# Optimization experiments

Hardware: AMD Instinct MI355X
Metric: run time of the kernel (lower is better)

The kernel has to match this reference:

```python
import jax, jax.numpy as jnp
import numpy as np

H = 128        # hidden_size
E = 128        # embedding_size
D = 2 * H      # num_directions * hidden_size
B = 512        # batch
T = 100        # n_cities == max_time_steps
MID = 100
STD = 0.1


def _p(k, shape):
    return STD * jax.random.normal(k, shape, dtype=jnp.float32)


def setup_inputs():
    ks = jax.random.split(jax.random.key(0), 22)
    return {
        "inputs": jax.random.normal(ks[0], (B, T, 2), dtype=jnp.float32),
        "W_embed": _p(ks[1], (E, 2)),
        "enc_Wih_f": _p(ks[2], (4 * H, E)),
        "enc_Whh_f": _p(ks[3], (4 * H, H)),
        "enc_b_f": _p(ks[4], (4 * H,)),
        "enc_Wih_b": _p(ks[5], (4 * H, E)),
        "enc_Whh_b": _p(ks[6], (4 * H, H)),
        "enc_b_b": _p(ks[7], (4 * H,)),
        "W_ref": _p(ks[8], (D, D)),
        "W_q": _p(ks[9], (D, D)),
        "v_w": _p(ks[10], (D,)),
        "v_b": _p(ks[11], (1,)),
        "proc_Wih_f": _p(ks[12], (4 * H, D)),
        "proc_Whh_f": _p(ks[13], (4 * H, H)),
        "proc_b_f": _p(ks[14], (4 * H,)),
        "proc_Wih_b": _p(ks[15], (4 * H, D)),
        "proc_Whh_b": _p(ks[16], (4 * H, H)),
        "proc_b_b": _p(ks[17], (4 * H,)),
        "W1": _p(ks[18], (MID, D)),
        "b1": _p(ks[19], (MID,)),
        "W2": _p(ks[20], (1, MID)),
        "b2": _p(ks[21], (1,)),
    }


def _cell(x, h, c, Wih, Whh, b):
    # PyTorch LSTM gate order: i, f, g, o
    gates = x @ Wih.T + h @ Whh.T + b
    i, f, g, o = jnp.split(gates, 4, axis=-1)
    c2 = jax.nn.sigmoid(f) * c + jax.nn.sigmoid(i) * jnp.tanh(g)
    h2 = jax.nn.sigmoid(o) * jnp.tanh(c2)
    return h2, c2


def _lstm_dir(xs, Wih, Whh, b):
    # xs: [T, B, in] -> (hs [T,B,H], h_last [B,H], c_last [B,H])
    bsz = xs.shape[1]
    h0 = jnp.zeros((bsz, H), xs.dtype)

    def step(carry, x):
        h, c = carry
        h, c = _cell(x, h, c, Wih, Whh, b)
        return (h, c), h

    (h, c), hs = jax.lax.scan(step, (h0, h0), xs)
    return hs, h, c


def _forward(inputs, W_embed, enc_Wih_f, enc_Whh_f, enc_b_f, enc_Wih_b, enc_Whh_b,
             enc_b_b, W_ref, W_q, v_w, v_b, proc_Wih_f, proc_Whh_f, proc_b_f,
             proc_Wih_b, proc_Whh_b, proc_b_b, W1, b1, W2, b2, remat=False):
    bsz, city, _ = inputs.shape
    emb = inputs @ W_embed.T                      # [B, T, E]
    xs = emb.transpose(1, 0, 2)                   # [T, B, E]
    hs_f, hf, cf = _lstm_dir(xs, enc_Wih_f, enc_Whh_f, enc_b_f)
    hs_b, hb, cb = _lstm_dir(xs[::-1], enc_Wih_b, enc_Whh_b, enc_b_b)
    enc = jnp.concatenate([hs_f, hs_b[::-1]], axis=-1).transpose(1, 0, 2)  # [B, T, D]
    ref = enc @ W_ref.T                           # loop-invariant W_ref(Enc): [B, T, D]

    def step(carry, _):
        pin, shf, scf, shb, scb = carry
        # bidirectional LSTM over a length-1 sequence = two independent cells
        shf, scf = _cell(pin, shf, scf, proc_Wih_f, proc_Whh_f, proc_b_f)
        shb, scb = _cell(pin, shb, scb, proc_Wih_b, proc_Whh_b, proc_b_b)
        pout = jnp.concatenate([shf, shb], axis=-1)              # [B, D]
        scores = jnp.tanh(ref + (pout @ W_q.T)[:, None, :]) @ v_w + v_b[0]  # [B, T]
        attn = jax.nn.softmax(scores, axis=1)
        pin = jnp.einsum('bt,btd->bd', attn, enc)                # glimpse
        return (pin, shf, scf, shb, scb), pout

    if remat:
        step = jax.checkpoint(step)

    pin0 = jnp.zeros((bsz, D), inputs.dtype)
    _, pouts = jax.lax.scan(step, (pin0, hf, cf, hb, cb), None, length=city)
    pout = pouts[-1]                              # processor_output of last step
    hidden = jax.nn.relu(pout @ W1.T + b1)
    return jnp.squeeze(hidden @ W2.T + b2)        # [B]


def reference(inputs, W_embed, enc_Wih_f, enc_Whh_f, enc_b_f, enc_Wih_b, enc_Whh_b,
              enc_b_b, W_ref, W_q, v_w, v_b, proc_Wih_f, proc_Whh_f, proc_b_f,
              proc_Wih_b, proc_Whh_b, proc_b_b, W1, b1, W2, b2):
    return _forward(inputs, W_embed, enc_Wih_f, enc_Whh_f, enc_b_f, enc_Wih_b,
                    enc_Whh_b, enc_b_b, W_ref, W_q, v_w, v_b, proc_Wih_f,
                    proc_Whh_f, proc_b_f, proc_Wih_b, proc_Whh_b, proc_b_b,
                    W1, b1, W2, b2)
```

## Files before the change

### kernel.cpp

```cpp
#include <hip/hip_runtime.h>


constexpr int kH = 128, kE = 128, kD = 256, kB = 512, kT = 100, kG = 512, kMID = 100;

typedef _Float16 half2_t __attribute__((ext_vector_type(2)));

constexpr size_t WS_ENCH  = 0;
constexpr size_t WS_REFTH = WS_ENCH  + (size_t)kB * kT * kD/2;
constexpr size_t WS_EW2   = WS_REFTH + (size_t)kB * kD * kT/2;
constexpr size_t WS_ECG   = WS_EW2   + 65536;
constexpr size_t WS_PW2   = WS_ECG   + 4096;
constexpr size_t WS_PB    = WS_PW2   + 196608;
constexpr size_t WS_WQ2   = WS_PB    + 1024;
constexpr size_t WS_WREFT = WS_WQ2   + 32768;
constexpr size_t WS_HST   = WS_WREFT + (size_t)kD * kD;
constexpr size_t WS_POUT  = WS_HST   + (size_t)4 * kB * kH;

__device__ __forceinline__ float rcpf(float x) { return __builtin_amdgcn_rcpf(x); }
__device__ __forceinline__ float sigf(float x) { return rcpf(1.0f + __expf(-x)); }
__device__ __forceinline__ float tanhf_(float x) {
    float t = __expf(2.0f * x);
    return 1.0f - 2.0f * rcpf(1.0f + t);
}
__device__ __forceinline__ float fdot2(half2_t a, half2_t b, float c) {
#if __has_builtin(__builtin_amdgcn_fdot2)
    return __builtin_amdgcn_fdot2(a, b, c, false);
#else
    return c + (float)a.x * (float)b.x + (float)a.y * (float)b.y;
#endif
}

__global__ void k_prep_ec(const float* __restrict__ Wih_f, const float* __restrict__ Wih_b,
                          const float* __restrict__ b_f, const float* __restrict__ b_b,
                          const float* __restrict__ Wemb, float* __restrict__ ws) {
    int id = blockIdx.x * 256 + threadIdx.x;
    int dir = id >> 9, j = id & 511;
    const float* Wih = dir ? Wih_b : Wih_f;
    const float* bb  = dir ? b_b   : b_f;
    float c0 = 0.f, c1 = 0.f;
    for (int e = 0; e < kE; ++e) {
        float w = Wih[j * kE + e];
        c0 += w * Wemb[e * 2 + 0];
        c1 += w * Wemb[e * 2 + 1];
    }
    float* ecg = ws + WS_ECG + (size_t)id * 4;
    ecg[0] = c0; ecg[1] = c1; ecg[2] = bb[j]; ecg[3] = 0.f;
}

__global__ void k_prep_tr(const float* __restrict__ eWhh_f, const float* __restrict__ eWhh_b,
                          const float* __restrict__ pWih_f, const float* __restrict__ pWih_b,
                          const float* __restrict__ pWhh_f, const float* __restrict__ pWhh_b,
                          const float* __restrict__ pb_f, const float* __restrict__ pb_b,
                          const float* __restrict__ Wq, const float* __restrict__ Wref,
                          float* __restrict__ ws) {
    int id = blockIdx.x * 256 + threadIdx.x;
    if (id < 65536) {
        int dir = id >> 15, rem = id & 32767, kp = rem >> 9, j = rem & 511;
        const float* W = dir ? eWhh_b : eWhh_f;
        half2_t v = {(_Float16)W[j * kH + 2 * kp], (_Float16)W[j * kH + 2 * kp + 1]};
        ((half2_t*)(ws + WS_EW2))[id] = v;
        return;
    }
    id -= 65536;
    if (id < 196608) {
        int kp = id >> 10, j = id & 1023;
        int k0 = 2 * kp, k1 = 2 * kp + 1;
        float a, b;
        if (k0 < 256) {
            a = (j < 512) ? pWih_f[j * kD + k0] : pWih_b[(j - 512) * kD + k0];
            b = (j < 512) ? pWih_f[j * kD + k1] : pWih_b[(j - 512) * kD + k1];
        } else {
            a = (j < 512) ? pWhh_f[j * kH + (k0 - 256)] : pWhh_b[(j - 512) * kH + (k0 - 256)];
            b = (j < 512) ? pWhh_f[j * kH + (k1 - 256)] : pWhh_b[(j - 512) * kH + (k1 - 256)];
        }
        half2_t v = {(_Float16)a, (_Float16)b};
        ((half2_t*)(ws + WS_PW2))[id] = v;
        return;
    }
    id -= 196608;
    if (id < 1024) {
        ws[WS_PB + id] = (id < 512) ? pb_f[id] : pb_b[id - 512];
        return;
    }
    id -= 1024;
    if (id < 32768) {
        int kp = id >> 8, n = id & 255;
        half2_t v = {(_Float16)Wq[n * kD + 2 * kp], (_Float16)Wq[n * kD + 2 * kp + 1]};
        ((half2_t*)(ws + WS_WQ2))[id] = v;
        return;
    }
    id -= 32768;
    if (id < 65536) {
        int k = id >> 8, n = id & 255;
        ws[WS_WREFT + id] = Wref[n * kD + k];
        return;
    }
}

__global__ __launch_bounds__(512, 2) void k_encoder(const float* __restrict__ inp,
                                                    float* __restrict__ ws) {
    const int dir = blockIdx.x & 1;
    const int b0  = (blockIdx.x >> 1) * 4;
    const int tid = threadIdx.x;
    const int jq  = tid & 127;
    const int kg  = tid >> 7;
    __shared__ __align__(16) half2_t shT2[64][4];
    __shared__ float scs[4][kH];
    __shared__ __align__(16) float uniE[4 * 4 * 512];
    __shared__ __align__(16) float4 secg[512];
    __shared__ float sx[4][2];
    if (tid < 256) ((float*)shT2)[tid] = 0.f;
    if (tid < 512) scs[tid >> 7][tid & 127] = 0.f;
    secg[tid] = *(const float4*)(ws + WS_ECG + (size_t)(dir * 512 + tid) * 4);
    const float4* EW2f4 = (const float4*)(ws + WS_EW2) + (size_t)dir * 64 * 128;
    _Float16* ench = (_Float16*)(ws + WS_ENCH);
    float* hst = ws + WS_HST;
    float4* uniE4 = (float4*)uniE;
    float4 wregE[16];
    #pragma unroll
    for (int i = 0; i < 16; ++i) wregE[i] = EW2f4[(kg * 16 + i) * 128 + jq];
    __syncthreads();
    for (int s = 0; s < kT; ++s) {
        const int t = dir ? (kT - 1 - s) : s;
        if (tid < 8) { int r = tid >> 1, c = tid & 1; sx[r][c] = inp[((size_t)(b0 + r) * kT + t) * 2 + c]; }
        {
            float aa[16];
            #pragma unroll
            for (int i = 0; i < 16; ++i) aa[i] = 0.f;
            #pragma unroll
            for (int kk = 0; kk < 16; ++kk) {
                int kp = kg * 16 + kk;
                float4 xraw = *(const float4*)&shT2[kp][0];
                const half2_t* wp = (const half2_t*)&wregE[kk];
                const half2_t* xp = (const half2_t*)&xraw;
                #pragma unroll
                for (int j = 0; j < 4; ++j)
                    #pragma unroll
                    for (int r = 0; r < 4; ++r)
                        aa[j * 4 + r] = fdot2(wp[j], xp[r], aa[j * 4 + r]);
            }
            #pragma unroll
            for (int r = 0; r < 4; ++r)
                uniE4[(kg * 4 + r) * 128 + jq] = make_float4(aa[0*4+r], aa[1*4+r], aa[2*4+r], aa[3*4+r]);
        }
        __syncthreads();
        {
            const int r = tid >> 7, k = tid & 127;
            float4 c0 = secg[k], c1 = secg[128 + k], c2 = secg[256 + k], c3 = secg[384 + k];
            float x0 = sx[r][0], x1 = sx[r][1];
            float gi = c0.z + x0 * c0.x + x1 * c0.y;
            float gf = c1.z + x0 * c1.x + x1 * c1.y;
            float gg = c2.z + x0 * c2.x + x1 * c2.y;
            float go = c3.z + x0 * c3.x + x1 * c3.y;
            #pragma unroll
            for (int g4 = 0; g4 < 4; ++g4) {
                const float* u = &uniE[(g4 * 4 + r) * 512];
                gi += u[k]; gf += u[k + 128]; gg += u[k + 256]; go += u[k + 384];
            }
            float cc = sigf(gf) * scs[r][k] + sigf(gi) * tanhf_(gg);
            float hh = sigf(go) * tanhf_(cc);
            scs[r][k] = cc;
            ((_Float16*)shT2)[((k >> 1) * 4 + r) * 2 + (k & 1)] = (_Float16)hh;
            ench[((size_t)(b0 + r) * kT + t) * kD + dir * kH + k] = (_Float16)hh;
            if (s == kT - 1) {
                hst[(size_t)(dir * 2 + 0) * kB * kH + (size_t)(b0 + r) * kH + k] = hh;
                hst[(size_t)(dir * 2 + 1) * kB * kH + (size_t)(b0 + r) * kH + k] = cc;
            }
        }
        __syncthreads();
    }
}

__global__ __launch_bounds__(256) void k_refgemm(float* __restrict__ ws) {
    const int tid = threadIdx.x;
    const int m0 = blockIdx.x * 20;
    const int b = m0 / kT, t0 = m0 % kT;
    __shared__ float se[20][kD];
    __shared__ float so[20][257];
    const _Float16* ench = (const _Float16*)(ws + WS_ENCH);
    const float* WrT = ws + WS_WREFT;
    _Float16* refTh = (_Float16*)(ws + WS_REFTH);
    #pragma unroll
    for (int i = 0; i < 20; ++i) se[i][tid] = (float)ench[(size_t)(m0 + i) * kD + tid];
    __syncthreads();
    float acc[20];
    #pragma unroll
    for (int r = 0; r < 20; ++r) acc[r] = 0.f;
    #pragma unroll 2
    for (int k = 0; k < kD; ++k) {
        float w = WrT[k * kD + tid];
        #pragma unroll
        for (int r = 0; r < 20; ++r) acc[r] += se[r][k] * w;
    }
    #pragma unroll
    for (int r = 0; r < 20; ++r) so[r][tid] = acc[r];
    __syncthreads();
    #pragma unroll
    for (int i = 0; i < 20; ++i) {
        int idx = i * 256 + tid;
        int d = idx / 20, tt = idx - d * 20;
        refTh[(size_t)b * kD * kT + d * kT + t0 + tt] = (_Float16)so[tt][d];
    }
}

__global__ __launch_bounds__(1024) void k_process(const float* __restrict__ vw,
                                                  const float* __restrict__ vb,
                                                  float* __restrict__ ws) {
    const int tid = threadIdx.x;
    const int b0 = blockIdx.x * 2;
    __shared__ __align__(16) half2_t xh2[2][192][2];
    __shared__ float pc[2][2][kH];
    __shared__ float hfp[2][2][kH];
    __shared__ __align__(16) float uni[8192];
    __shared__ float qv[2][kD];
    __shared__ float at[2][128];
    __shared__ float vwS[kD];
    __shared__ float sbias[1024];
    const float* PB   = ws + WS_PB;
    const _Float16* refTh = (const _Float16*)(ws + WS_REFTH);
    const _Float16* ench  = (const _Float16*)(ws + WS_ENCH);
    const float* hst  = ws + WS_HST;
    const float4* PW2f4 = (const float4*)(ws + WS_PW2);
    const float*  WQ2f  = ws + WS_WQ2;
    _Float16* xf = (_Float16*)xh2;
    if (tid < 512) {
        int zjh = tid >> 8, zkp = (tid >> 1) & 127, zr = tid & 1;
        ((float*)xh2)[(zjh * 192 + zkp) * 2 + zr] = 0.f;
    }
    if (tid < 512) {
        int r = tid >> 8, dirk = tid & 255, dir = dirk >> 7, k = dirk & 127;
        float hv = hst[(size_t)(dir * 2 + 0) * kB * kH + (size_t)(b0 + r) * kH + k];
        pc[dir][r][k]  = hst[(size_t)(dir * 2 + 1) * kB * kH + (size_t)(b0 + r) * kH + k];
        hfp[dir][r][k] = hv;
        xf[((dir * 192 + 128 + (k >> 1)) * 2 + r) * 2 + (k & 1)] = (_Float16)hv;
    }
    if (tid < kD) vwS[tid] = vw[tid];
    sbias[tid] = PB[tid];
    const float vbias = vb[0];
    const int jq = tid & 255;
    const int kg = tid >> 8;
    const int jh = (jq >= 128);
    float4* uni4 = (float4*)uni;
    __syncthreads();

    for (int step = 0; step < kT; ++step) {
        {
            float a00=0,a01=0,a02=0,a03=0, a10=0,a11=0,a12=0,a13=0;
            #pragma unroll 8
            for (int kk = 0; kk < 48; ++kk) {
                int kp = kg * 48 + kk;
                float4 wraw = PW2f4[(size_t)kp * 256 + jq];
                float2 xraw = *(const float2*)&xh2[jh][kp][0];
                const half2_t* wp = (const half2_t*)&wraw;
                const half2_t* xp = (const half2_t*)&xraw;
                a00 = fdot2(wp[0], xp[0], a00); a01 = fdot2(wp[1], xp[0], a01);
                a02 = fdot2(wp[2], xp[0], a02); a03 = fdot2(wp[3], xp[0], a03);
                a10 = fdot2(wp[0], xp[1], a10); a11 = fdot2(wp[1], xp[1], a11);
                a12 = fdot2(wp[2], xp[1], a12); a13 = fdot2(wp[3], xp[1], a13);
            }
            uni4[(kg * 2 + 0) * 256 + jq] = make_float4(a00,a01,a02,a03);
            uni4[(kg * 2 + 1) * 256 + jq] = make_float4(a10,a11,a12,a13);
        }
        __syncthreads();
        if (tid < 512) {
            int r = tid >> 8, dirk = tid & 255, dir = dirk >> 7, k = dirk & 127;
            int base = dir * 512;
            int j0 = base + k, j1 = base + 128 + k, j2 = base + 256 + k, j3 = base + 384 + k;
            float gi = sbias[j0], gf = sbias[j1], gg = sbias[j2], go = sbias[j3];
            #pragma unroll
            for (int g4 = 0; g4 < 4; ++g4) {
                const float* u = &uni[(g4 * 2 + r) * 1024];
                gi += u[j0]; gf += u[j1]; gg += u[j2]; go += u[j3];
            }
            float cc = sigf(gf) * pc[dir][r][k] + sigf(gi) * tanhf_(gg);
            float hh = sigf(go) * tanhf_(cc);
            pc[dir][r][k] = cc; hfp[dir][r][k] = hh;
            xf[((dir * 192 + 128 + (k >> 1)) * 2 + r) * 2 + (k & 1)] = (_Float16)hh;
        }
        __syncthreads();
        if (step < kT - 1) {
            {
                int n = tid & 255, kh = tid >> 8;
                float q0 = 0.f, q1 = 0.f;
                #pragma unroll 8
                for (int i = 0; i < 32; ++i) {
                    int kp = kh * 32 + i;
                    int dir = kp >> 6, lkp = kp & 63;
                    float wr = WQ2f[kp * 256 + n];
                    float2 xraw = *(const float2*)&xh2[dir][128 + lkp][0];
                    const half2_t* xp = (const half2_t*)&xraw;
                    half2_t w = *(const half2_t*)&wr;
                    q0 = fdot2(w, xp[0], q0);
                    q1 = fdot2(w, xp[1], q1);
                }
                uni[(kh * 2 + 0) * 256 + n] = q0;
                uni[(kh * 2 + 1) * 256 + n] = q1;
            }
            __syncthreads();
            if (tid < 512) {
                int r = tid >> 8, n = tid & 255;
                float q = 0.f;
                #pragma unroll
                for (int kh = 0; kh < 4; ++kh) q += uni[(kh * 2 + r) * 256 + n];
                qv[r][n] = q;
            }
            __syncthreads();
            if (tid < 800) {
                int r = tid / 400, rem = tid - r * 400;
                int dg = rem / 50, tp = rem - dg * 50;
                const _Float16* rbase = refTh + ((size_t)(b0 + r) * kD + dg * 32) * kT + 2 * tp;
                float acc0 = 0.f, acc1 = 0.f;
                #pragma unroll 8
                for (int i = 0; i < 32; ++i) {
                    int d = dg * 32 + i;
                    half2_t rv = *(const half2_t*)(rbase + (size_t)i * kT);
                    float qd = qv[r][d], w = vwS[d];
                    acc0 += w * tanhf_((float)rv.x + qd);
                    acc1 += w * tanhf_((float)rv.y + qd);
                }
                uni[(r * 8 + dg) * 100 + 2 * tp]     = acc0;
                uni[(r * 8 + dg) * 100 + 2 * tp + 1] = acc1;
            }
            __syncthreads();
            {
                int wv = tid >> 6, l = tid & 63;
                if (wv < 2) {
                    int r = wv;
                    float s1 = vbias, s2 = -3.0e38f;
                    #pragma unroll
                    for (int g = 0; g < 8; ++g) s1 += uni[(r * 8 + g) * 100 + l];
                    if (l + 64 < kT) {
                        s2 = vbias;
                        #pragma unroll
                        for (int g = 0; g < 8; ++g) s2 += uni[(r * 8 + g) * 100 + l + 64];
                    }
                    float m = fmaxf(s1, s2);
                    #pragma unroll
                    for (int off = 32; off > 0; off >>= 1) m = fmaxf(m, __shfl_xor(m, off));
                    float e1 = __expf(s1 - m);
                    float e2 = (l + 64 < kT) ? __expf(s2 - m) : 0.f;
                    float ssum = e1 + e2;
                    #pragma unroll
                    for (int off = 32; off > 0; off >>= 1) ssum += __shfl_xor(ssum, off);
                    float inv = rcpf(ssum);
                    at[r][l] = e1 * inv;
                    at[r][l + 64] = e2 * inv;
                }
            }
            __syncthreads();
            {
                int dp = tid & 127, r = (tid >> 7) & 1, th = tid >> 8;
                const half2_t* erow = (const half2_t*)(ench + ((size_t)(b0 + r) * kT + th * 25) * kD) + dp;
                float a0 = 0.f, a1 = 0.f;
                #pragma unroll 5
                for (int i = 0; i < 25; ++i) {
                    half2_t e = erow[(size_t)i * (kD / 2)];
                    float w = at[r][th * 25 + i];
                    a0 += w * (float)e.x;
                    a1 += w * (float)e.y;
                }
                uni[(th * 2 + r) * 256 + 2 * dp]     = a0;
                uni[(th * 2 + r) * 256 + 2 * dp + 1] = a1;
            }
            __syncthreads();
            if (tid < 512) {
                int r = tid >> 8, d = tid & 255;
                float v = 0.f;
                #pragma unroll
                for (int th = 0; th < 4; ++th) v += uni[(th * 2 + r) * 256 + d];
                _Float16 hv = (_Float16)v;
                xf[((0 * 192 + (d >> 1)) * 2 + r) * 2 + (d & 1)] = hv;
                xf[((1 * 192 + (d >> 1)) * 2 + r) * 2 + (d & 1)] = hv;
            }
            __syncthreads();
        }
    }
    float* pout = ws + WS_POUT;
    if (tid < 512) {
        int r = tid >> 8, d = tid & 255;
        pout[(size_t)(b0 + r) * kD + d] = (d < 128) ? hfp[0][r][d] : hfp[1][r][d - 128];
    }
}

__global__ __launch_bounds__(128) void k_mlp(const float* __restrict__ W1, const float* __restrict__ b1,
                                             const float* __restrict__ W2, const float* __restrict__ b2,
                                             const float* __restrict__ ws, float* __restrict__ out) {
    const int tid = threadIdx.x;
    const int b0 = blockIdx.x * 4;
    __shared__ float sp[4][kD];
    __shared__ float hid[4][kMID];
    const float* pout = ws + WS_POUT;
    #pragma unroll
    for (int i = 0; i < 8; ++i) {
        int f = i * 128 + tid;
        int r = f >> 8, k = f & 255;
        sp[r][k] = pout[(size_t)(b0 + r) * kD + k];
    }
    __syncthreads();
    if (tid < kMID) {
        int m = tid;
        #pragma unroll
        for (int r = 0; r < 4; ++r) {
            float acc = b1[m];
            for (int k = 0; k < kD; ++k) acc += sp[r][k] * W1[m * kD + k];
            hid[r][m] = fmaxf(acc, 0.f);
        }
    }
    __syncthreads();
    if (tid < 4) {
        float acc = b2[0];
        for (int m = 0; m < kMID; ++m) acc += hid[tid][m] * W2[m];
        out[b0 + tid] = acc;
    }
}

extern "C" void kernel_launch(void* const* d_in, const int* in_sizes, int n_in,
                              void* d_out, int out_size, void* d_ws, size_t ws_size,
                              hipStream_t stream) {
    (void)in_sizes; (void)n_in; (void)out_size; (void)ws_size;
    const float* inp    = (const float*)d_in[0];
    const float* Wemb   = (const float*)d_in[1];
    const float* eWih_f = (const float*)d_in[2];
    const float* eWhh_f = (const float*)d_in[3];
    const float* eb_f   = (const float*)d_in[4];
    const float* eWih_b = (const float*)d_in[5];
    const float* eWhh_b = (const float*)d_in[6];
    const float* eb_b   = (const float*)d_in[7];
    const float* Wref   = (const float*)d_in[8];
    const float* Wq     = (const float*)d_in[9];
    const float* vw     = (const float*)d_in[10];
    const float* vb     = (const float*)d_in[11];
    const float* pWih_f = (const float*)d_in[12];
    const float* pWhh_f = (const float*)d_in[13];
    const float* pb_f   = (const float*)d_in[14];
    const float* pWih_b = (const float*)d_in[15];
    const float* pWhh_b = (const float*)d_in[16];
    const float* pb_b   = (const float*)d_in[17];
    const float* W1     = (const float*)d_in[18];
    const float* b1     = (const float*)d_in[19];
    const float* W2     = (const float*)d_in[20];
    const float* b2     = (const float*)d_in[21];
    float* ws  = (float*)d_ws;
    float* out = (float*)d_out;

    k_prep_ec<<<4, 256, 0, stream>>>(eWih_f, eWih_b, eb_f, eb_b, Wemb, ws);
    k_prep_tr<<<1412, 256, 0, stream>>>(eWhh_f, eWhh_b, pWih_f, pWih_b,
                                        pWhh_f, pWhh_b, pb_f, pb_b, Wq, Wref, ws);
    k_encoder<<<256, 512, 0, stream>>>(inp, ws);
    k_refgemm<<<2560, 256, 0, stream>>>(ws);
    k_process<<<256, 1024, 0, stream>>>(vw, vb, ws);
    k_mlp<<<128, 128, 0, stream>>>(W1, b1, W2, b2, ws, out);
}
```

Baseline: 2.159 ms.

## Prefetch weights and ref rows across phases, drop split-K reductions in processor loop

Prefetches the first 8 rows of the LSTM gate weights into registers during the previous step's glimpse phase, and the first 16 ref elements before the query matvec, so global loads overlap other work. The query matvec and glimpse sum change from a 4-way split-K with a shared-memory reduction to a single thread per output looping over all K. This removes two barriers per step. The cost is higher register pressure, idle threads (only 512 of the 1024 work in those phases) and longer serial loops per thread.

```diff
diff --git a/kernel.cpp b/kernel.cpp
--- a/kernel.cpp
+++ b/kernel.cpp
@@ -241,22 +241,51 @@
     const int kg = tid >> 8;
     const int jh = (jq >= 128);
     float4* uni4 = (float4*)uni;
+    const int r6 = tid / 400;
+    const int rem6 = tid - r6 * 400;
+    const int dg6 = rem6 / 50, tp6 = rem6 - dg6 * 50;
+    const _Float16* rbase6 = refTh + ((size_t)(b0 + r6) * kD + dg6 * 32) * kT + 2 * tp6;
+    float4 wpre[8];
+    #pragma unroll
+    for (int i = 0; i < 8; ++i) wpre[i] = PW2f4[(size_t)(kg * 48 + i) * 256 + jq];
     __syncthreads();
 
     for (int step = 0; step < kT; ++step) {
         {
             float a00=0,a01=0,a02=0,a03=0, a10=0,a11=0,a12=0,a13=0;
-            #pragma unroll 8
-            for (int kk = 0; kk < 48; ++kk) {
-                int kp = kg * 48 + kk;
-                float4 wraw = PW2f4[(size_t)kp * 256 + jq];
-                float2 xraw = *(const float2*)&xh2[jh][kp][0];
-                const half2_t* wp = (const half2_t*)&wraw;
-                const half2_t* xp = (const half2_t*)&xraw;
-                a00 = fdot2(wp[0], xp[0], a00); a01 = fdot2(wp[1], xp[0], a01);
-                a02 = fdot2(wp[2], xp[0], a02); a03 = fdot2(wp[3], xp[0], a03);
-                a10 = fdot2(wp[0], xp[1], a10); a11 = fdot2(wp[1], xp[1], a11);
-                a12 = fdot2(wp[2], xp[1], a12); a13 = fdot2(wp[3], xp[1], a13);
+            #pragma unroll
+            for (int p = 0; p < 4; ++p) {
+                int kp = kg * 48 + 2 * p;
+                float4 x2 = *(const float4*)&xh2[jh][kp][0];
+                const half2_t* xp = (const half2_t*)&x2;
+                const half2_t* w0 = (const half2_t*)&wpre[2 * p];
+                const half2_t* w1 = (const half2_t*)&wpre[2 * p + 1];
+                a00 = fdot2(w0[0], xp[0], a00); a01 = fdot2(w0[1], xp[0], a01);
+                a02 = fdot2(w0[2], xp[0], a02); a03 = fdot2(w0[3], xp[0], a03);
+                a10 = fdot2(w0[0], xp[1], a10); a11 = fdot2(w0[1], xp[1], a11);
+                a12 = fdot2(w0[2], xp[1], a12); a13 = fdot2(w0[3], xp[1], a13);
+                a00 = fdot2(w1[0], xp[2], a00); a01 = fdot2(w1[1], xp[2], a01);
+                a02 = fdot2(w1[2], xp[2], a02); a03 = fdot2(w1[3], xp[2], a03);
+                a10 = fdot2(w1[0], xp[3], a10); a11 = fdot2(w1[1], xp[3], a11);
+                a12 = fdot2(w1[2], xp[3], a12); a13 = fdot2(w1[3], xp[3], a13);
+            }
+            #pragma unroll 4
+            for (int p = 0; p < 20; ++p) {
+                int kp = kg * 48 + 8 + 2 * p;
+                float4 wraw0 = PW2f4[(size_t)kp * 256 + jq];
+                float4 wraw1 = PW2f4[(size_t)(kp + 1) * 256 + jq];
+                float4 x2 = *(const float4*)&xh2[jh][kp][0];
+                const half2_t* xp = (const half2_t*)&x2;
+                const half2_t* w0 = (const half2_t*)&wraw0;
+                const half2_t* w1 = (const half2_t*)&wraw1;
+                a00 = fdot2(w0[0], xp[0], a00); a01 = fdot2(w0[1], xp[0], a01);
+                a02 = fdot2(w0[2], xp[0], a02); a03 = fdot2(w0[3], xp[0], a03);
+                a10 = fdot2(w0[0], xp[1], a10); a11 = fdot2(w0[1], xp[1], a11);
+                a12 = fdot2(w0[2], xp[1], a12); a13 = fdot2(w0[3], xp[1], a13);
+                a00 = fdot2(w1[0], xp[2], a00); a01 = fdot2(w1[1], xp[2], a01);
+                a02 = fdot2(w1[2], xp[2], a02); a03 = fdot2(w1[3], xp[2], a03);
+                a10 = fdot2(w1[0], xp[3], a10); a11 = fdot2(w1[1], xp[3], a11);
+                a12 = fdot2(w1[2], xp[3], a12); a13 = fdot2(w1[3], xp[3], a13);
             }
             uni4[(kg * 2 + 0) * 256 + jq] = make_float4(a00,a01,a02,a03);
             uni4[(kg * 2 + 1) * 256 + jq] = make_float4(a10,a11,a12,a13);
@@ -279,47 +308,39 @@
         }
         __syncthreads();
         if (step < kT - 1) {
-            {
-                int n = tid & 255, kh = tid >> 8;
-                float q0 = 0.f, q1 = 0.f;
+            half2_t rpre[16];
+            if (tid < 800) {
+                #pragma unroll
+                for (int i = 0; i < 16; ++i)
+                    rpre[i] = *(const half2_t*)(rbase6 + (size_t)i * kT);
+            }
+            if (tid < 512) {
+                int n = tid & 255, r = tid >> 8;
+                float q = 0.f;
                 #pragma unroll 8
-                for (int i = 0; i < 32; ++i) {
-                    int kp = kh * 32 + i;
+                for (int kp = 0; kp < 128; ++kp) {
                     int dir = kp >> 6, lkp = kp & 63;
                     float wr = WQ2f[kp * 256 + n];
-                    float2 xraw = *(const float2*)&xh2[dir][128 + lkp][0];
-                    const half2_t* xp = (const half2_t*)&xraw;
+                    half2_t x = xh2[dir][128 + lkp][r];
                     half2_t w = *(const half2_t*)&wr;
-                    q0 = fdot2(w, xp[0], q0);
-                    q1 = fdot2(w, xp[1], q1);
+                    q = fdot2(w, x, q);
                 }
-                uni[(kh * 2 + 0) * 256 + n] = q0;
-                uni[(kh * 2 + 1) * 256 + n] = q1;
-            }
-            __syncthreads();
-            if (tid < 512) {
-                int r = tid >> 8, n = tid & 255;
-                float q = 0.f;
-                #pragma unroll
-                for (int kh = 0; kh < 4; ++kh) q += uni[(kh * 2 + r) * 256 + n];
                 qv[r][n] = q;
             }
             __syncthreads();
             if (tid < 800) {
-                int r = tid / 400, rem = tid - r * 400;
-                int dg = rem / 50, tp = rem - dg * 50;
-                const _Float16* rbase = refTh + ((size_t)(b0 + r) * kD + dg * 32) * kT + 2 * tp;
                 float acc0 = 0.f, acc1 = 0.f;
                 #pragma unroll 8
                 for (int i = 0; i < 32; ++i) {
-                    int d = dg * 32 + i;
-                    half2_t rv = *(const half2_t*)(rbase + (size_t)i * kT);
-                    float qd = qv[r][d], w = vwS[d];
+                    int d = dg6 * 32 + i;
+                    half2_t rv = (i < 16) ? rpre[i]
+                               : *(const half2_t*)(rbase6 + (size_t)i * kT);
+                    float qd = qv[r6][d], w = vwS[d];
                     acc0 += w * tanhf_((float)rv.x + qd);
                     acc1 += w * tanhf_((float)rv.y + qd);
                 }
-                uni[(r * 8 + dg) * 100 + 2 * tp]     = acc0;
-                uni[(r * 8 + dg) * 100 + 2 * tp + 1] = acc1;
+                uni[(r6 * 8 + dg6) * 100 + 2 * tp6]     = acc0;
+                uni[(r6 * 8 + dg6) * 100 + 2 * tp6 + 1] = acc1;
             }
             __syncthreads();
             {
@@ -349,28 +370,20 @@
             }
             __syncthreads();
             {
-                int dp = tid & 127, r = (tid >> 7) & 1, th = tid >> 8;
-                const half2_t* erow = (const half2_t*)(ench + ((size_t)(b0 + r) * kT + th * 25) * kD) + dp;
-                float a0 = 0.f, a1 = 0.f;
-                #pragma unroll 5
-                for (int i = 0; i < 25; ++i) {
-                    half2_t e = erow[(size_t)i * (kD / 2)];
-                    float w = at[r][th * 25 + i];
-                    a0 += w * (float)e.x;
-                    a1 += w * (float)e.y;
+                #pragma unroll
+                for (int i = 0; i < 8; ++i)
+                    wpre[i] = PW2f4[(size_t)(kg * 48 + i) * 256 + jq];
+                if (tid < 512) {
+                    int r = tid >> 8, d = tid & 255;
+                    const _Float16* erow = ench + (size_t)(b0 + r) * kT * kD + d;
+                    float acc = 0.f;
+                    #pragma unroll 4
+                    for (int t = 0; t < kT; ++t)
+                        acc += at[r][t] * (float)erow[(size_t)t * kD];
+                    _Float16 hv = (_Float16)acc;
+                    xf[((0 * 192 + (d >> 1)) * 2 + r) * 2 + (d & 1)] = hv;
+                    xf[((1 * 192 + (d >> 1)) * 2 + r) * 2 + (d & 1)] = hv;
                 }
-                uni[(th * 2 + r) * 256 + 2 * dp]     = a0;
-                uni[(th * 2 + r) * 256 + 2 * dp + 1] = a1;
-            }
-            __syncthreads();
-            if (tid < 512) {
-                int r = tid >> 8, d = tid & 255;
-                float v = 0.f;
-                #pragma unroll
-                for (int th = 0; th < 4; ++th) v += uni[(th * 2 + r) * 256 + d];
-                _Float16 hv = (_Float16)v;
-                xf[((0 * 192 + (d >> 1)) * 2 + r) * 2 + (d & 1)] = hv;
-                xf[((1 * 192 + (d >> 1)) * 2 + r) * 2 + (d & 1)] = hv;
             }
             __syncthreads();
         }
```

Result: slower. 3.219 ms (+49.1%).
